# Performance work log

Hardware: AMD Instinct MI355X
Metric: run time of the kernel (lower is better)

The kernel has to match this reference:

```python
import jax, jax.numpy as jnp
import numpy as np

N = 100000          # nodes
E = 1600000         # edges (avg degree 16)
IN_DIM = 128
OUT_DIM = 128
H = 4               # num_heads
D = OUT_DIM // H    # per-head dim = 32
R = 64              # num relations
NEG_SLOPE = 0.2     # DGL GATConv default


def setup_inputs() -> dict:
    key = jax.random.key(0)
    ks = jax.random.split(key, 9)
    h = jax.random.normal(ks[0], (N, IN_DIM), dtype=jnp.float32)
    src = jax.random.randint(ks[1], (E,), 0, N, dtype=jnp.int32)
    dst = jax.random.randint(ks[2], (E,), 0, N, dtype=jnp.int32)
    rel_types = jax.random.randint(ks[3], (E,), 0, R, dtype=jnp.int32)
    # learned params (GATConv fc weight, attention vectors, bias; relation embedding)
    W = jax.random.normal(ks[4], (H * D, IN_DIM), dtype=jnp.float32) * 0.1
    attn_l = jax.random.normal(ks[5], (H, D), dtype=jnp.float32) * 0.1
    attn_r = jax.random.normal(ks[6], (H, D), dtype=jnp.float32) * 0.1
    bias = jax.random.normal(ks[7], (H * D,), dtype=jnp.float32) * 0.01
    rel_emb = jax.random.normal(ks[8], (R, IN_DIM), dtype=jnp.float32) * 0.1
    return {"h": h, "src": src, "dst": dst, "rel_types": rel_types,
            "W": W, "attn_l": attn_l, "attn_r": attn_r, "bias": bias,
            "rel_emb": rel_emb}


def reference(h, src, dst, rel_types, W, attn_l, attn_r, bias, rel_emb):
    # NOTE: the original module builds edata 'e' = h[src] + rel_emb[rel_types],
    # but DGL's GATConv never reads it, so it does not affect the output.
    # Eval mode: feat_drop / attn_drop disabled (deterministic reference).

    # GATConv: project and split heads. [N, H, D]
    feat = (h @ W.T).reshape(N, H, D)
    # per-node attention logits: a_l^T Wh_i, a_r^T Wh_j  -> [N, H]
    el = (feat * attn_l).sum(-1)
    er = (feat * attn_r).sum(-1)
    # per-edge score e_ij = LeakyReLU(el[src] + er[dst])  -> [E, H]
    e = jax.nn.leaky_relu(el[src] + er[dst], NEG_SLOPE)
    # segment softmax over incoming edges of each destination node
    m = jax.ops.segment_max(e, dst, num_segments=N)           # [N, H]
    a = jnp.exp(e - m[dst])                                    # [E, H]
    denom = jax.ops.segment_sum(a, dst, num_segments=N)       # [N, H]
    alpha = a / denom[dst]                                     # [E, H]
    # weighted scatter-aggregate of source features
    msg = feat[src] * alpha[:, :, None]                        # [E, H, D]
    out = jax.ops.segment_sum(msg, dst, num_segments=N)       # [N, H, D]
    out = out + bias.reshape(1, H, D)
    # mean over heads -> [N, D]
    return out.mean(axis=1)
```

## Files before the change

### kernel.cpp

```cpp
#include <hip/hip_runtime.h>
#include <math.h>

#define NEG_SLOPE 0.2f

static __device__ __forceinline__ float bf2f(unsigned int hw) {
    return __uint_as_float(hw << 16);
}
static __device__ __forceinline__ unsigned short f2bf(float f) {
    unsigned int u = __float_as_uint(f);
    u += 0x7FFFu + ((u >> 16) & 1u);
    return (unsigned short)(u >> 16);
}

__global__ __launch_bounds__(256, 3) void k_gemm_hist(
    const float* __restrict__ h, const float* __restrict__ W,
    unsigned short* __restrict__ featp, int N,
    const int* __restrict__ dst, int* __restrict__ cnt, int* __restrict__ pos,
    int E, int gemm_blocks)
{
    __shared__ float As[64 * 68];
    __shared__ float Bs[128 * 64];

    if (blockIdx.x >= gemm_blocks) {
        int e = (blockIdx.x - gemm_blocks) * 512 + threadIdx.x;
        if (e < E) pos[e] = atomicAdd(&cnt[dst[e]], 1);
        e += 256;
        if (e < E) pos[e] = atomicAdd(&cnt[dst[e]], 1);
        return;
    }

    const int tid = threadIdx.x;
    const int rb = blockIdx.x * 64;
    const int tc = tid & 31;
    const int tr = tid >> 5;

    float acc[8][4];
#pragma unroll
    for (int i = 0; i < 8; ++i)
#pragma unroll
        for (int j = 0; j < 4; ++j) acc[i][j] = 0.0f;

    for (int kch = 0; kch < 2; ++kch) {
        if (kch) __syncthreads();
#pragma unroll
        for (int i = 0; i < 4; ++i) {
            int chunk = i * 256 + tid;
            int r = chunk >> 4;
            int kc = (chunk & 15) << 2;
            int row = rb + r;
            float4 v = make_float4(0.f, 0.f, 0.f, 0.f);
            if (row < N) v = *(const float4*)(h + (size_t)row * 128 + kch * 64 + kc);
            *(float4*)(As + r * 68 + kc) = v;
        }
#pragma unroll
        for (int i = 0; i < 8; ++i) {
            int chunk = i * 256 + tid;
            int c = chunk >> 4;
            int kc = (chunk & 15) << 2;
            float4 v = *(const float4*)(W + (size_t)c * 128 + kch * 64 + kc);
            int slot = (kc >> 2) ^ (c & 7);
            *(float4*)(Bs + (c << 6) + (slot << 2)) = v;
        }
        __syncthreads();

#pragma unroll 4
        for (int k4 = 0; k4 < 64; k4 += 4) {
            float4 b[4];
#pragma unroll
            for (int j = 0; j < 4; ++j) {
                int c = tc + 32 * j;
                int slot = (k4 >> 2) ^ (c & 7);
                b[j] = *(const float4*)(Bs + (c << 6) + (slot << 2));
            }
            float4 a[8];
#pragma unroll
            for (int i = 0; i < 8; ++i)
                a[i] = *(const float4*)(As + (tr * 8 + i) * 68 + k4);
#pragma unroll
            for (int i = 0; i < 8; ++i)
#pragma unroll
                for (int j = 0; j < 4; ++j)
                    acc[i][j] += a[i].x * b[j].x + a[i].y * b[j].y +
                                 a[i].z * b[j].z + a[i].w * b[j].w;
        }
    }
#pragma unroll
    for (int i = 0; i < 8; ++i) {
        int row = rb + tr * 8 + i;
        if (row < N) {
            ushort4 pk;
            pk.x = f2bf(acc[i][0]);
            pk.y = f2bf(acc[i][1]);
            pk.z = f2bf(acc[i][2]);
            pk.w = f2bf(acc[i][3]);
            *(ushort4*)(featp + (size_t)row * 128 + tc * 4) = pk;
        }
    }
}

__global__ void k_scan1(const int* __restrict__ cnt, int* __restrict__ bsum, int N) {
    __shared__ int sd[256];
    int t = threadIdx.x;
    int i = blockIdx.x * 256 + t;
    sd[t] = (i < N) ? cnt[i] : 0;
    __syncthreads();
    for (int s = 128; s > 0; s >>= 1) {
        if (t < s) sd[t] += sd[t + s];
        __syncthreads();
    }
    if (t == 0) bsum[blockIdx.x] = sd[0];
}

__global__ void k_scan2(int* __restrict__ bsum, int nb) {
    __shared__ int sd[1024];
    int t = threadIdx.x;
    sd[t] = (t < nb) ? bsum[t] : 0;
    __syncthreads();
    for (int off = 1; off < 1024; off <<= 1) {
        int add = (t >= off) ? sd[t - off] : 0;
        __syncthreads();
        sd[t] += add;
        __syncthreads();
    }
    if (t < nb) bsum[t] = (t == 0) ? 0 : sd[t - 1];
}

__global__ void k_scan3(const int* __restrict__ cnt, const int* __restrict__ bsum,
                        int* __restrict__ row, int N) {
    __shared__ int sd[256];
    int t = threadIdx.x;
    int i = blockIdx.x * 256 + t;
    int v = (i < N) ? cnt[i] : 0;
    sd[t] = v;
    __syncthreads();
    for (int off = 1; off < 256; off <<= 1) {
        int add = (t >= off) ? sd[t - off] : 0;
        __syncthreads();
        sd[t] += add;
        __syncthreads();
    }
    if (i < N) row[i] = bsum[blockIdx.x] + sd[t] - v;
}

__global__ void k_scatter_elr(const int* __restrict__ src, const int* __restrict__ dst,
                              const int* __restrict__ pos, const int* __restrict__ row,
                              int* __restrict__ esrc, int E, int scat_blocks,
                              const unsigned short* __restrict__ featp,
                              const float* __restrict__ attn_l,
                              const float* __restrict__ attn_r,
                              float* __restrict__ el, float* __restrict__ er, int N) {
    if (blockIdx.x < scat_blocks) {
        int e = blockIdx.x * 512 + threadIdx.x;
        if (e < E) esrc[row[dst[e]] + pos[e]] = src[e];
        e += 256;
        if (e < E) esrc[row[dst[e]] + pos[e]] = src[e];
        return;
    }
    int g = (blockIdx.x - scat_blocks) * 256 + threadIdx.x;
    int node = g >> 5;
    int d = g & 31;
    if (node >= N) return;
    uint2 u = *(const uint2*)(featp + (size_t)node * 128 + d * 4);
    float f0 = bf2f(u.x & 0xffffu);
    float f1 = bf2f(u.x >> 16);
    float f2 = bf2f(u.y & 0xffffu);
    float f3 = bf2f(u.y >> 16);
    float pl0 = f0 * attn_l[d],      pr0 = f0 * attn_r[d];
    float pl1 = f1 * attn_l[32 + d], pr1 = f1 * attn_r[32 + d];
    float pl2 = f2 * attn_l[64 + d], pr2 = f2 * attn_r[64 + d];
    float pl3 = f3 * attn_l[96 + d], pr3 = f3 * attn_r[96 + d];
#pragma unroll
    for (int m = 1; m < 32; m <<= 1) {
        pl0 += __shfl_xor(pl0, m); pr0 += __shfl_xor(pr0, m);
        pl1 += __shfl_xor(pl1, m); pr1 += __shfl_xor(pr1, m);
        pl2 += __shfl_xor(pl2, m); pr2 += __shfl_xor(pr2, m);
        pl3 += __shfl_xor(pl3, m); pr3 += __shfl_xor(pr3, m);
    }
    if (d == 0) {
        *(float4*)(el + (size_t)node * 4) = make_float4(pl0, pl1, pl2, pl3);
        *(float4*)(er + (size_t)node * 4) = make_float4(pr0, pr1, pr2, pr3);
    }
}

__global__ __launch_bounds__(256) void k_pull(const int* __restrict__ esrc,
                                              const int* __restrict__ row,
                                              const int* __restrict__ cnt,
                                              const float* __restrict__ el,
                                              const float* __restrict__ er,
                                              const unsigned short* __restrict__ featp,
                                              const float* __restrict__ bias,
                                              float* __restrict__ out, int N) {
    int wave = (int)((blockIdx.x * (size_t)blockDim.x + threadIdx.x) >> 6);
    if (wave >= N) return;
    int lane = threadIdx.x & 63;
    int half = lane >> 5;
    int d = lane & 31;
    int start = row[wave];
    int deg = cnt[wave];
    float4 r4 = *(const float4*)(er + 4 * (size_t)wave);

    float acc0 = 0.f, acc1 = 0.f, acc2 = 0.f, acc3 = 0.f;
    float dn0 = 0.f, dn1 = 0.f, dn2 = 0.f, dn3 = 0.f;

    for (int base = 0; base < deg; base += 64) {
        int m = deg - base;
        if (m > 64) m = 64;
        int s_mine = 0;
        float a0 = 0.f, a1 = 0.f, a2 = 0.f, a3 = 0.f;
        if (lane < m) {
            s_mine = esrc[start + base + lane];
            float4 l4 = *(const float4*)(el + 4 * (size_t)s_mine);
            float v0 = l4.x + r4.x; v0 = v0 > 0.f ? v0 : NEG_SLOPE * v0;
            float v1 = l4.y + r4.y; v1 = v1 > 0.f ? v1 : NEG_SLOPE * v1;
            float v2 = l4.z + r4.z; v2 = v2 > 0.f ? v2 : NEG_SLOPE * v2;
            float v3 = l4.w + r4.w; v3 = v3 > 0.f ? v3 : NEG_SLOPE * v3;
            a0 = __expf(v0); a1 = __expf(v1); a2 = __expf(v2); a3 = __expf(v3);
            dn0 += a0; dn1 += a1; dn2 += a2; dn3 += a3;
        }
        for (int ii = 0; ii < m; ii += 2) {
            int i = ii + half;
            int sj   = __shfl(s_mine, i);
            float b0 = __shfl(a0, i);
            float b1 = __shfl(a1, i);
            float b2 = __shfl(a2, i);
            float b3 = __shfl(a3, i);
            uint2 u = *(const uint2*)(featp + (size_t)sj * 128 + d * 4);
            float f0 = bf2f(u.x & 0xffffu);
            float f1 = bf2f(u.x >> 16);
            float f2 = bf2f(u.y & 0xffffu);
            float f3 = bf2f(u.y >> 16);
            acc0 += b0 * f0; acc1 += b1 * f1; acc2 += b2 * f2; acc3 += b3 * f3;
        }
    }
    acc0 += __shfl_xor(acc0, 32); acc1 += __shfl_xor(acc1, 32);
    acc2 += __shfl_xor(acc2, 32); acc3 += __shfl_xor(acc3, 32);
#pragma unroll
    for (int m = 1; m < 64; m <<= 1) {
        dn0 += __shfl_xor(dn0, m); dn1 += __shfl_xor(dn1, m);
        dn2 += __shfl_xor(dn2, m); dn3 += __shfl_xor(dn3, m);
    }
    if (half == 0) {
        float msum = 0.f;
        if (dn0 > 0.f)
            msum = acc0 / dn0 + acc1 / dn1 + acc2 / dn2 + acc3 / dn3;
        float b = 0.25f * (bias[d] + bias[32 + d] + bias[64 + d] + bias[96 + d]);
        out[(size_t)wave * 32 + d] = 0.25f * msum + b;
    }
}

extern "C" void kernel_launch(void* const* d_in, const int* in_sizes, int n_in,
                              void* d_out, int out_size, void* d_ws, size_t ws_size,
                              hipStream_t stream) {
    const float* h      = (const float*)d_in[0];
    const int*   src    = (const int*)d_in[1];
    const int*   dst    = (const int*)d_in[2];
    const float* W      = (const float*)d_in[4];
    const float* attn_l = (const float*)d_in[5];
    const float* attn_r = (const float*)d_in[6];
    const float* bias   = (const float*)d_in[7];
    float* out = (float*)d_out;

    const int N = in_sizes[0] / 128;
    const int E = in_sizes[1];

    float* el = (float*)d_ws;
    float* er = el + (size_t)N * 4;
    unsigned short* featp = (unsigned short*)(er + (size_t)N * 4);
    int* cnt  = (int*)(featp + (size_t)N * 128);
    int* row  = cnt + N;
    int* bsum = row + N;
    int* pos  = bsum + 1024;
    int* esrc = pos + E;
    int nb = (N + 255) / 256;

    hipMemsetAsync(cnt, 0, (size_t)N * 4, stream);

    int gemm_blocks = (N + 63) / 64;
    int hist_blocks = (E + 511) / 512;
    k_gemm_hist<<<gemm_blocks + hist_blocks, 256, 0, stream>>>(
        h, W, featp, N, dst, cnt, pos, E, gemm_blocks);

    k_scan1<<<nb, 256, 0, stream>>>(cnt, bsum, N);
    k_scan2<<<1, 1024, 0, stream>>>(bsum, nb);
    k_scan3<<<nb, 256, 0, stream>>>(cnt, bsum, row, N);

    int scat_blocks = (E + 511) / 512;
    int elr_blocks = ((size_t)N * 32 + 255) / 256;
    k_scatter_elr<<<scat_blocks + elr_blocks, 256, 0, stream>>>(
        src, dst, pos, row, esrc, E, scat_blocks,
        featp, attn_l, attn_r, el, er, N);

    k_pull<<<((size_t)N * 64 + 255) / 256, 256, 0, stream>>>(esrc, row, cnt, el, er,
                                                             featp, bias, out, N);
}
```

Baseline: 351.4 us.

## Store GEMM tiles as bf16 in LDS, raise occupancy, reorder hist blocks

```diff
diff --git a/kernel.cpp b/kernel.cpp
--- a/kernel.cpp
+++ b/kernel.cpp
@@ -5,6 +5,12 @@
 
 static __device__ __forceinline__ float bf2f(unsigned int hw) {
     return __uint_as_float(hw << 16);
+}
+static __device__ __forceinline__ float bf2f_lo(unsigned int u) {
+    return __uint_as_float(u << 16);
+}
+static __device__ __forceinline__ float bf2f_hi(unsigned int u) {
+    return __uint_as_float(u & 0xffff0000u);
 }
 static __device__ __forceinline__ unsigned short f2bf(float f) {
     unsigned int u = __float_as_uint(f);
@@ -12,25 +18,27 @@
     return (unsigned short)(u >> 16);
 }
 
-__global__ __launch_bounds__(256, 3) void k_gemm_hist(
+__global__ __launch_bounds__(256, 5) void k_gemm_hist(
     const float* __restrict__ h, const float* __restrict__ W,
     unsigned short* __restrict__ featp, int N,
     const int* __restrict__ dst, int* __restrict__ cnt, int* __restrict__ pos,
-    int E, int gemm_blocks)
+    int E, int hist_blocks)
 {
-    __shared__ float As[64 * 68];
-    __shared__ float Bs[128 * 64];
-
-    if (blockIdx.x >= gemm_blocks) {
-        int e = (blockIdx.x - gemm_blocks) * 512 + threadIdx.x;
-        if (e < E) pos[e] = atomicAdd(&cnt[dst[e]], 1);
-        e += 256;
-        if (e < E) pos[e] = atomicAdd(&cnt[dst[e]], 1);
+    __shared__ unsigned short As[64 * 68];
+    __shared__ unsigned short Bs[128 * 64];
+
+    if (blockIdx.x < hist_blocks) {
+        int t0 = blockIdx.x * 2048 + threadIdx.x;
+#pragma unroll
+        for (int q = 0; q < 8; ++q) {
+            int e = t0 + q * 256;
+            if (e < E) pos[e] = atomicAdd(&cnt[dst[e]], 1);
+        }
         return;
     }
 
     const int tid = threadIdx.x;
-    const int rb = blockIdx.x * 64;
+    const int rb = (blockIdx.x - hist_blocks) * 64;
     const int tc = tid & 31;
     const int tr = tid >> 5;
 
@@ -50,7 +58,9 @@
             int row = rb + r;
             float4 v = make_float4(0.f, 0.f, 0.f, 0.f);
             if (row < N) v = *(const float4*)(h + (size_t)row * 128 + kch * 64 + kc);
-            *(float4*)(As + r * 68 + kc) = v;
+            ushort4 pk;
+            pk.x = f2bf(v.x); pk.y = f2bf(v.y); pk.z = f2bf(v.z); pk.w = f2bf(v.w);
+            *(ushort4*)(As + r * 68 + kc) = pk;
         }
 #pragma unroll
         for (int i = 0; i < 8; ++i) {
@@ -58,30 +68,34 @@
             int c = chunk >> 4;
             int kc = (chunk & 15) << 2;
             float4 v = *(const float4*)(W + (size_t)c * 128 + kch * 64 + kc);
-            int slot = (kc >> 2) ^ (c & 7);
-            *(float4*)(Bs + (c << 6) + (slot << 2)) = v;
+            ushort4 pk;
+            pk.x = f2bf(v.x); pk.y = f2bf(v.y); pk.z = f2bf(v.z); pk.w = f2bf(v.w);
+            int slot = (kc >> 2) ^ (c & 15);
+            *(ushort4*)(Bs + (c << 6) + (slot << 2)) = pk;
         }
         __syncthreads();
 
 #pragma unroll 4
         for (int k4 = 0; k4 < 64; k4 += 4) {
-            float4 b[4];
+            float bx[4][4];
 #pragma unroll
             for (int j = 0; j < 4; ++j) {
                 int c = tc + 32 * j;
-                int slot = (k4 >> 2) ^ (c & 7);
-                b[j] = *(const float4*)(Bs + (c << 6) + (slot << 2));
+                int slot = (k4 >> 2) ^ (c & 15);
+                uint2 u = *(const uint2*)(Bs + (c << 6) + (slot << 2));
+                bx[j][0] = bf2f_lo(u.x); bx[j][1] = bf2f_hi(u.x);
+                bx[j][2] = bf2f_lo(u.y); bx[j][3] = bf2f_hi(u.y);
             }
-            float4 a[8];
-#pragma unroll
-            for (int i = 0; i < 8; ++i)
-                a[i] = *(const float4*)(As + (tr * 8 + i) * 68 + k4);
-#pragma unroll
-            for (int i = 0; i < 8; ++i)
+#pragma unroll
+            for (int i = 0; i < 8; ++i) {
+                uint2 u = *(const uint2*)(As + (tr * 8 + i) * 68 + k4);
+                float a0 = bf2f_lo(u.x), a1 = bf2f_hi(u.x);
+                float a2 = bf2f_lo(u.y), a3 = bf2f_hi(u.y);
 #pragma unroll
                 for (int j = 0; j < 4; ++j)
-                    acc[i][j] += a[i].x * b[j].x + a[i].y * b[j].y +
-                                 a[i].z * b[j].z + a[i].w * b[j].w;
+                    acc[i][j] += a0 * bx[j][0] + a1 * bx[j][1] +
+                                 a2 * bx[j][2] + a3 * bx[j][3];
+            }
         }
     }
 #pragma unroll
@@ -161,10 +175,10 @@
     int d = g & 31;
     if (node >= N) return;
     uint2 u = *(const uint2*)(featp + (size_t)node * 128 + d * 4);
-    float f0 = bf2f(u.x & 0xffffu);
-    float f1 = bf2f(u.x >> 16);
-    float f2 = bf2f(u.y & 0xffffu);
-    float f3 = bf2f(u.y >> 16);
+    float f0 = bf2f_lo(u.x);
+    float f1 = bf2f_hi(u.x);
+    float f2 = bf2f_lo(u.y);
+    float f3 = bf2f_hi(u.y);
     float pl0 = f0 * attn_l[d],      pr0 = f0 * attn_r[d];
     float pl1 = f1 * attn_l[32 + d], pr1 = f1 * attn_r[32 + d];
     float pl2 = f2 * attn_l[64 + d], pr2 = f2 * attn_r[64 + d];
@@ -225,10 +239,10 @@
             float b2 = __shfl(a2, i);
             float b3 = __shfl(a3, i);
             uint2 u = *(const uint2*)(featp + (size_t)sj * 128 + d * 4);
-            float f0 = bf2f(u.x & 0xffffu);
-            float f1 = bf2f(u.x >> 16);
-            float f2 = bf2f(u.y & 0xffffu);
-            float f3 = bf2f(u.y >> 16);
+            float f0 = bf2f_lo(u.x);
+            float f1 = bf2f_hi(u.x);
+            float f2 = bf2f_lo(u.y);
+            float f3 = bf2f_hi(u.y);
             acc0 += b0 * f0; acc1 += b1 * f1; acc2 += b2 * f2; acc3 += b3 * f3;
         }
     }
@@ -275,10 +289,10 @@
 
     hipMemsetAsync(cnt, 0, (size_t)N * 4, stream);
 
+    int hist_blocks = (E + 2047) / 2048;
     int gemm_blocks = (N + 63) / 64;
-    int hist_blocks = (E + 511) / 512;
-    k_gemm_hist<<<gemm_blocks + hist_blocks, 256, 0, stream>>>(
-        h, W, featp, N, dst, cnt, pos, E, gemm_blocks);
+    k_gemm_hist<<<hist_blocks + gemm_blocks, 256, 0, stream>>>(
+        h, W, featp, N, dst, cnt, pos, E, hist_blocks);
 
     k_scan1<<<nb, 256, 0, stream>>>(cnt, bsum, N);
     k_scan2<<<1, 1024, 0, stream>>>(bsum, nb);
```

After: 669.4 us. +90.5%, slower.
